# Performance work log

Hardware: AMD Instinct MI355X
Metric: run time of the kernel (lower is better)

Reference implementation:

```python
import jax, jax.numpy as jnp
import numpy as np

DIM = 4096
NUM_EXPERTS = 64
TOP_K = 2
BATCH = 4
SEQ = 4096


def setup_inputs() -> dict:
    key = jax.random.key(0)
    kx, kw = jax.random.split(key)
    x = jax.random.normal(kx, (BATCH, SEQ, DIM), dtype=jnp.float32)
    # nn.Linear(dim, num_experts, bias=False) -> weight [num_experts, dim]
    W = jax.random.normal(kw, (NUM_EXPERTS, DIM), dtype=jnp.float32) * (1.0 / np.sqrt(DIM))
    return {"x": x, "W": W}


def reference(x, W):
    # router logits: [B, S, E]
    router_logits = jnp.einsum('bsd,ed->bse', x, W)
    # top-k selection over experts
    top_k_logits, expert_indices = jax.lax.top_k(router_logits, TOP_K)
    expert_weights = jax.nn.softmax(top_k_logits, axis=-1)        # [B, S, K]
    routing_probs = jax.nn.softmax(router_logits, axis=-1)        # [B, S, E]
    expert_usage = routing_probs.mean(axis=(0, 1))                # [E]
    load_balance_loss = (expert_usage * expert_usage).sum() * NUM_EXPERTS
    router_z_loss = (jax.nn.logsumexp(router_logits, axis=-1) ** 2).mean()
    return (expert_weights, expert_indices, load_balance_loss,
            router_z_loss, expert_usage, routing_probs)
```

## Files before the change

kernel.cpp:

```cpp
#include <hip/hip_runtime.h>
#include <math.h>

#define DIM      4096
#define NE       64
#define M_TOK    16384
#define BM       64
#define BK       32
#define LDS_LD   66

__global__ __launch_bounds__(256) void gemm_logits(
    const float* __restrict__ x, const float* __restrict__ W,
    float* __restrict__ part0, float* __restrict__ wsp, int kQ)
{
    const int mt  = blockIdx.x;
    const int ks  = blockIdx.y;
    const int tid = threadIdx.x;
    const int tx  = tid & 15;
    const int ty  = tid >> 4;
    const int tok0 = mt * BM;
    const int k0   = ks * kQ;

    __shared__ float Xs[BK][LDS_LD];
    __shared__ float Ws[BK][LDS_LD];

    float acc[4][4] = {};

    for (int kt = k0; kt < k0 + kQ; kt += BK) {
        #pragma unroll
        for (int j = 0; j < 2; ++j) {
            const int f   = tid + 256 * j;
            const int row = f >> 3;
            const int c4  = f & 7;
            const float4 xv = *reinterpret_cast<const float4*>(
                &x[(size_t)(tok0 + row) * DIM + kt + c4 * 4]);
            Xs[c4 * 4 + 0][row] = xv.x;
            Xs[c4 * 4 + 1][row] = xv.y;
            Xs[c4 * 4 + 2][row] = xv.z;
            Xs[c4 * 4 + 3][row] = xv.w;
            const float4 wv = *reinterpret_cast<const float4*>(
                &W[(size_t)row * DIM + kt + c4 * 4]);
            Ws[c4 * 4 + 0][row] = wv.x;
            Ws[c4 * 4 + 1][row] = wv.y;
            Ws[c4 * 4 + 2][row] = wv.z;
            Ws[c4 * 4 + 3][row] = wv.w;
        }
        __syncthreads();

        #pragma unroll
        for (int kk = 0; kk < BK; ++kk) {
            float a[4], b[4];
            #pragma unroll
            for (int i = 0; i < 4; ++i) a[i] = Xs[kk][ty * 4 + i];
            #pragma unroll
            for (int j = 0; j < 4; ++j) b[j] = Ws[kk][tx * 4 + j];
            #pragma unroll
            for (int i = 0; i < 4; ++i)
                #pragma unroll
                for (int j = 0; j < 4; ++j)
                    acc[i][j] = fmaf(a[i], b[j], acc[i][j]);
        }
        __syncthreads();
    }

    float* outp = (ks == 0) ? part0 : (wsp + (size_t)(ks - 1) * (M_TOK * NE));
    #pragma unroll
    for (int i = 0; i < 4; ++i) {
        const size_t off = (size_t)(tok0 + ty * 4 + i) * NE + tx * 4;
        *reinterpret_cast<float2*>(&outp[off])     = make_float2(acc[i][0], acc[i][1]);
        *reinterpret_cast<float2*>(&outp[off + 2]) = make_float2(acc[i][2], acc[i][3]);
    }
}

__global__ __launch_bounds__(256) void epilogue(
    float* probs_logits, const float* __restrict__ wsp, int KS,
    float* __restrict__ out_w, float* __restrict__ out_idx,
    float* __restrict__ out_usage, float* __restrict__ z_acc)
{
    const int tid  = threadIdx.x;
    const int lane = tid & 63;
    const int w    = tid >> 6;
    const int tok0 = blockIdx.x * 64;

    float local_usage = 0.f;
    float local_z     = 0.f;

    for (int i = 0; i < 16; ++i) {
        const int t = tok0 + w * 16 + i;
        const size_t base = (size_t)t * NE + lane;
        float v = probs_logits[base];
        for (int s = 1; s < KS; ++s)
            v += wsp[(size_t)(s - 1) * (M_TOK * NE) + base];

        float m = v; int mi = lane;
        #pragma unroll
        for (int off = 32; off >= 1; off >>= 1) {
            const float om = __shfl_xor(m, off);
            const int   oi = __shfl_xor(mi, off);
            if (om > m || (om == m && oi < mi)) { m = om; mi = oi; }
        }
        const float m1 = m; const int i1 = mi;

        float m2 = (lane == i1) ? -INFINITY : v; int mi2 = lane;
        #pragma unroll
        for (int off = 32; off >= 1; off >>= 1) {
            const float om = __shfl_xor(m2, off);
            const int   oi = __shfl_xor(mi2, off);
            if (om > m2 || (om == m2 && oi < mi2)) { m2 = om; mi2 = oi; }
        }

        const float e = expf(v - m1);
        float s = e;
        #pragma unroll
        for (int off = 32; off >= 1; off >>= 1) s += __shfl_xor(s, off);
        const float p = e / s;
        probs_logits[base] = p;
        local_usage += p;

        const float lse = m1 + logf(s);
        local_z += lse * lse;

        if (lane == 0) {
            const float d   = expf(m2 - m1);
            const float inv = 1.f / (1.f + d);
            out_w[t * 2]     = inv;
            out_w[t * 2 + 1] = d * inv;
            out_idx[t * 2]     = (float)i1;
            out_idx[t * 2 + 1] = (float)mi2;
        }
    }

    __shared__ float us[4][NE];
    __shared__ float zs[4];
    us[w][lane] = local_usage;
    if (lane == 0) zs[w] = local_z;
    __syncthreads();
    if (tid < NE) {
        const float su = us[0][tid] + us[1][tid] + us[2][tid] + us[3][tid];
        atomicAdd(&out_usage[tid], su);
    }
    if (tid == 0) atomicAdd(z_acc, zs[0] + zs[1] + zs[2] + zs[3]);
}

__global__ void finalize(float* usage, float* lb, float* z)
{
    const int e = threadIdx.x;
    const float u = usage[e] * (1.f / (float)M_TOK);
    usage[e] = u;
    float s = u * u;
    #pragma unroll
    for (int off = 32; off >= 1; off >>= 1) s += __shfl_xor(s, off);
    if (e == 0) {
        lb[0] = s * (float)NE;
        z[0]  = z[0] * (1.f / (float)M_TOK);
    }
}

extern "C" void kernel_launch(void* const* d_in, const int* in_sizes, int n_in,
                              void* d_out, int out_size, void* d_ws, size_t ws_size,
                              hipStream_t stream)
{
    const float* x = (const float*)d_in[0];
    const float* W = (const float*)d_in[1];
    float* o = (float*)d_out;

    float* out_w     = o;
    float* out_idx   = o + 32768;
    float* out_lb    = o + 65536;
    float* out_z     = o + 65537;
    float* out_usage = o + 65538;
    float* out_probs = o + 65602;

    const size_t partBytes = (size_t)M_TOK * NE * sizeof(float);
    int KS = 1;
    if      (ws_size >= 7 * partBytes) KS = 8;
    else if (ws_size >= 3 * partBytes) KS = 4;
    else if (ws_size >= 1 * partBytes) KS = 2;

    hipMemsetAsync(out_z, 0, 65 * sizeof(float), stream);

    dim3 g1(M_TOK / BM, KS);
    gemm_logits<<<g1, 256, 0, stream>>>(x, W, out_probs, (float*)d_ws, DIM / KS);
    epilogue<<<M_TOK / 64, 256, 0, stream>>>(out_probs, (const float*)d_ws, KS,
                                             out_w, out_idx, out_usage, out_z);
    finalize<<<1, 64, 0, stream>>>(out_usage, out_lb, out_z);
}
```

Before: 497.2 us.

## Fuse router GEMM with softmax/top-k epilogue and double-buffer LDS tiles

Replaces the split-K GEMM plus separate epilogue with one kernel per 64-token tile that accumulates over the full hidden dimension. Logits are staged in shared memory and reduced in-block, which removes the workspace partial-sum writes and reads and a kernel launch. Global loads are prefetched into registers and written to a second LDS buffer, and inner-loop LDS reads use float4. In exchange, the grid shrinks to 256 blocks with no split-K, which reduces parallelism and latency hiding on a memory-bound stream over x.

Result: slower. 514.7 us (+3.5%).

```diff
diff --git a/kernel.cpp b/kernel.cpp
--- a/kernel.cpp
+++ b/kernel.cpp
@@ -1,95 +1,108 @@
 #include <hip/hip_runtime.h>
 #include <math.h>
 
-#define DIM      4096
-#define NE       64
-#define M_TOK    16384
-#define BM       64
-#define BK       32
-#define LDS_LD   66
+#define DIM    4096
+#define NE     64
+#define M_TOK  16384
+#define BK     32
+#define LD     68
 
-__global__ __launch_bounds__(256) void gemm_logits(
+__global__ __launch_bounds__(256) void moe_fused(
     const float* __restrict__ x, const float* __restrict__ W,
-    float* __restrict__ part0, float* __restrict__ wsp, int kQ)
+    float* __restrict__ out_w, float* __restrict__ out_idx,
+    float* __restrict__ out_usage, float* __restrict__ z_acc,
+    float* __restrict__ out_probs)
 {
-    const int mt  = blockIdx.x;
-    const int ks  = blockIdx.y;
-    const int tid = threadIdx.x;
-    const int tx  = tid & 15;
-    const int ty  = tid >> 4;
-    const int tok0 = mt * BM;
-    const int k0   = ks * kQ;
+    __shared__ float Xs[2][BK][LD];
+    __shared__ float Ws[2][BK][LD];
+    __shared__ float Ls[64][LD];
+    __shared__ float us[4][NE];
+    __shared__ float zs[4];
 
-    __shared__ float Xs[BK][LDS_LD];
-    __shared__ float Ws[BK][LDS_LD];
+    const int tid  = threadIdx.x;
+    const int tx   = tid & 15;
+    const int ty   = tid >> 4;
+    const int tok0 = blockIdx.x * 64;
+
+    const int srow = tid >> 3;
+    const int sc4  = tid & 7;
+    const float* xbase = x + (size_t)(tok0 + srow) * DIM + sc4 * 4;
+    const float* wbase = W + (size_t)srow * DIM + sc4 * 4;
 
     float acc[4][4] = {};
 
-    for (int kt = k0; kt < k0 + kQ; kt += BK) {
+    {
+        const float4 xv0 = *(const float4*)(xbase);
+        const float4 xv1 = *(const float4*)(xbase + 32 * DIM);
+        const float4 wv0 = *(const float4*)(wbase);
+        const float4 wv1 = *(const float4*)(wbase + 32 * DIM);
         #pragma unroll
-        for (int j = 0; j < 2; ++j) {
-            const int f   = tid + 256 * j;
-            const int row = f >> 3;
-            const int c4  = f & 7;
-            const float4 xv = *reinterpret_cast<const float4*>(
-                &x[(size_t)(tok0 + row) * DIM + kt + c4 * 4]);
-            Xs[c4 * 4 + 0][row] = xv.x;
-            Xs[c4 * 4 + 1][row] = xv.y;
-            Xs[c4 * 4 + 2][row] = xv.z;
-            Xs[c4 * 4 + 3][row] = xv.w;
-            const float4 wv = *reinterpret_cast<const float4*>(
-                &W[(size_t)row * DIM + kt + c4 * 4]);
-            Ws[c4 * 4 + 0][row] = wv.x;
-            Ws[c4 * 4 + 1][row] = wv.y;
-            Ws[c4 * 4 + 2][row] = wv.z;
-            Ws[c4 * 4 + 3][row] = wv.w;
+        for (int q = 0; q < 4; ++q) {
+            Xs[0][sc4 * 4 + q][srow]      = ((const float*)&xv0)[q];
+            Xs[0][sc4 * 4 + q][srow + 32] = ((const float*)&xv1)[q];
+            Ws[0][sc4 * 4 + q][srow]      = ((const float*)&wv0)[q];
+            Ws[0][sc4 * 4 + q][srow + 32] = ((const float*)&wv1)[q];
         }
-        __syncthreads();
+    }
+    __syncthreads();
+
+    int buf = 0;
+    for (int kt = 0; kt < DIM; kt += BK) {
+        float4 xv0, xv1, wv0, wv1;
+        const bool next = (kt + BK) < DIM;
+        if (next) {
+            const float* xp = xbase + kt + BK;
+            const float* wp = wbase + kt + BK;
+            xv0 = *(const float4*)(xp);
+            xv1 = *(const float4*)(xp + 32 * DIM);
+            wv0 = *(const float4*)(wp);
+            wv1 = *(const float4*)(wp + 32 * DIM);
+        }
 
         #pragma unroll
         for (int kk = 0; kk < BK; ++kk) {
-            float a[4], b[4];
-            #pragma unroll
-            for (int i = 0; i < 4; ++i) a[i] = Xs[kk][ty * 4 + i];
-            #pragma unroll
-            for (int j = 0; j < 4; ++j) b[j] = Ws[kk][tx * 4 + j];
+            const float4 a4 = *(const float4*)&Xs[buf][kk][ty * 4];
+            const float4 b4 = *(const float4*)&Ws[buf][kk][tx * 4];
+            const float a[4] = {a4.x, a4.y, a4.z, a4.w};
+            const float b[4] = {b4.x, b4.y, b4.z, b4.w};
             #pragma unroll
             for (int i = 0; i < 4; ++i)
                 #pragma unroll
                 for (int j = 0; j < 4; ++j)
                     acc[i][j] = fmaf(a[i], b[j], acc[i][j]);
         }
+
+        if (next) {
+            const int nb = buf ^ 1;
+            #pragma unroll
+            for (int q = 0; q < 4; ++q) {
+                Xs[nb][sc4 * 4 + q][srow]      = ((const float*)&xv0)[q];
+                Xs[nb][sc4 * 4 + q][srow + 32] = ((const float*)&xv1)[q];
+                Ws[nb][sc4 * 4 + q][srow]      = ((const float*)&wv0)[q];
+                Ws[nb][sc4 * 4 + q][srow + 32] = ((const float*)&wv1)[q];
+            }
+        }
         __syncthreads();
+        buf ^= 1;
     }
 
-    float* outp = (ks == 0) ? part0 : (wsp + (size_t)(ks - 1) * (M_TOK * NE));
     #pragma unroll
     for (int i = 0; i < 4; ++i) {
-        const size_t off = (size_t)(tok0 + ty * 4 + i) * NE + tx * 4;
-        *reinterpret_cast<float2*>(&outp[off])     = make_float2(acc[i][0], acc[i][1]);
-        *reinterpret_cast<float2*>(&outp[off + 2]) = make_float2(acc[i][2], acc[i][3]);
+        *(float4*)&Ls[ty * 4 + i][tx * 4] =
+            make_float4(acc[i][0], acc[i][1], acc[i][2], acc[i][3]);
     }
-}
+    __syncthreads();
 
-__global__ __launch_bounds__(256) void epilogue(
-    float* probs_logits, const float* __restrict__ wsp, int KS,
-    float* __restrict__ out_w, float* __restrict__ out_idx,
-    float* __restrict__ out_usage, float* __restrict__ z_acc)
-{
-    const int tid  = threadIdx.x;
     const int lane = tid & 63;
     const int w    = tid >> 6;
-    const int tok0 = blockIdx.x * 64;
 
     float local_usage = 0.f;
     float local_z     = 0.f;
 
     for (int i = 0; i < 16; ++i) {
-        const int t = tok0 + w * 16 + i;
-        const size_t base = (size_t)t * NE + lane;
-        float v = probs_logits[base];
-        for (int s = 1; s < KS; ++s)
-            v += wsp[(size_t)(s - 1) * (M_TOK * NE) + base];
+        const int tl = w * 16 + i;
+        const int t  = tok0 + tl;
+        const float v = Ls[tl][lane];
 
         float m = v; int mi = lane;
         #pragma unroll
@@ -113,7 +126,7 @@
         #pragma unroll
         for (int off = 32; off >= 1; off >>= 1) s += __shfl_xor(s, off);
         const float p = e / s;
-        probs_logits[base] = p;
+        out_probs[(size_t)t * NE + lane] = p;
         local_usage += p;
 
         const float lse = m1 + logf(s);
@@ -122,15 +135,13 @@
         if (lane == 0) {
             const float d   = expf(m2 - m1);
             const float inv = 1.f / (1.f + d);
-            out_w[t * 2]     = inv;
-            out_w[t * 2 + 1] = d * inv;
+            out_w[t * 2]       = inv;
+            out_w[t * 2 + 1]   = d * inv;
             out_idx[t * 2]     = (float)i1;
             out_idx[t * 2 + 1] = (float)mi2;
         }
     }
 
-    __shared__ float us[4][NE];
-    __shared__ float zs[4];
     us[w][lane] = local_usage;
     if (lane == 0) zs[w] = local_z;
     __syncthreads();
@@ -170,17 +181,9 @@
     float* out_usage = o + 65538;
     float* out_probs = o + 65602;
 
-    const size_t partBytes = (size_t)M_TOK * NE * sizeof(float);
-    int KS = 1;
-    if      (ws_size >= 7 * partBytes) KS = 8;
-    else if (ws_size >= 3 * partBytes) KS = 4;
-    else if (ws_size >= 1 * partBytes) KS = 2;
-
     hipMemsetAsync(out_z, 0, 65 * sizeof(float), stream);
 
-    dim3 g1(M_TOK / BM, KS);
-    gemm_logits<<<g1, 256, 0, stream>>>(x, W, out_probs, (float*)d_ws, DIM / KS);
-    epilogue<<<M_TOK / 64, 256, 0, stream>>>(out_probs, (const float*)d_ws, KS,
-                                             out_w, out_idx, out_usage, out_z);
+    moe_fused<<<M_TOK / 64, 256, 0, stream>>>(x, W, out_w, out_idx,
+                                              out_usage, out_z, out_probs);
     finalize<<<1, 64, 0, stream>>>(out_usage, out_lb, out_z);
 }
```
